# Kernel tuning notes

Measured on AMD Instinct MI355X. Metric: run time of the kernel, lower is better.

Reference implementation:

```python
import jax, jax.numpy as jnp
import numpy as np

N_NODES = 50000
N_EDGES = 640000
D_IN = 128
D_HID = 128
D_OUT = 128
N_GRAPHS = 64


def gcn_conv(x, edge_index, W, b, n_nodes):
    """PyG GCNConv: D^{-1/2} (A + I) D^{-1/2} X W + b (unit edge weights)."""
    src, dst = edge_index[0], edge_index[1]
    h = x @ W  # [N, d_out]
    # degree counts target-side edges plus the self loop
    deg = jax.ops.segment_sum(jnp.ones_like(dst, dtype=h.dtype), dst,
                              num_segments=n_nodes) + 1.0
    dinv = jax.lax.rsqrt(deg)  # deg >= 1 so always finite
    norm = dinv[src] * dinv[dst]  # [E]
    msg = h[src] * norm[:, None]  # gather + scale  [E, d_out]
    agg = jax.ops.segment_sum(msg, dst, num_segments=n_nodes)
    # self-loop contribution: norm_ii = dinv_i^2
    agg = agg + h * (dinv * dinv)[:, None]
    return agg + b


def global_mean_pool(x, batch, n_graphs):
    sums = jax.ops.segment_sum(x, batch, num_segments=n_graphs)
    cnt = jax.ops.segment_sum(jnp.ones((x.shape[0],), dtype=x.dtype), batch,
                              num_segments=n_graphs)
    return sums / jnp.maximum(cnt, 1.0)[:, None]


def setup_inputs() -> dict:
    key = jax.random.key(0)
    k = jax.random.split(key, 8)
    x = jax.random.normal(k[0], (N_NODES, D_IN), dtype=jnp.float32)
    edge_index = jax.random.randint(k[1], (2, N_EDGES), 0, N_NODES, dtype=jnp.int64)
    batch = jnp.sort(jax.random.randint(k[2], (N_NODES,), 0, N_GRAPHS, dtype=jnp.int64))
    s1 = 1.0 / np.sqrt(D_IN)
    s2 = 1.0 / np.sqrt(D_HID)
    W1 = jax.random.uniform(k[3], (D_IN, D_HID), jnp.float32, -s1, s1)
    b1 = jnp.zeros((D_HID,), jnp.float32)
    W2 = jax.random.uniform(k[4], (D_HID, D_OUT), jnp.float32, -s2, s2)
    b2 = jnp.zeros((D_OUT,), jnp.float32)
    return {"x": x, "edge_index": edge_index, "batch": batch,
            "W1": W1, "b1": b1, "W2": W2, "b2": b2}


def reference(x, edge_index, batch, W1, b1, W2, b2):
    n = x.shape[0]
    h = jax.nn.relu(gcn_conv(x, edge_index, W1, b1, n))
    h = gcn_conv(h, edge_index, W2, b2, n)
    return global_mean_pool(h, batch, N_GRAPHS)
```

## Files before the change

### kernel.cpp

```cpp
#include <hip/hip_runtime.h>


#define D 128
#define NGRAPH 64
#define AGG_BLOCKS 2048
#define BUCK_SH 9
#define BUCK_W  512
#define MAXBUCK 128

typedef _Float16 h16x2 __attribute__((ext_vector_type(2)));
typedef _Float16 f16x8 __attribute__((ext_vector_type(8)));
typedef float    f32x4 __attribute__((ext_vector_type(4)));
typedef unsigned short u16x8 __attribute__((ext_vector_type(8)));

__device__ __forceinline__ float2 h2f(unsigned u) {
    h16x2 h = __builtin_bit_cast(h16x2, u);
    return make_float2((float)h.x, (float)h.y);
}
__device__ __forceinline__ unsigned f2h(float x, float y) {
    h16x2 h;
    h.x = (_Float16)x;
    h.y = (_Float16)y;
    return __builtin_bit_cast(unsigned, h);
}
__device__ __forceinline__ void fmix2(float& ax, float& ay, unsigned u) {
    h16x2 h = __builtin_bit_cast(h16x2, u);
#if __has_builtin(__builtin_amdgcn_fdot2)
    const h16x2 onelo = {(_Float16)1.0f, (_Float16)0.0f};
    const h16x2 onehi = {(_Float16)0.0f, (_Float16)1.0f};
    ax = __builtin_amdgcn_fdot2(h, onelo, ax, false);
    ay = __builtin_amdgcn_fdot2(h, onehi, ay, false);
#else
    ax += (float)h.x;
    ay += (float)h.y;
#endif
}

__global__ void zero_out_kernel(float* __restrict__ out, int n) {
    int i = blockIdx.x * blockDim.x + threadIdx.x;
    if (i < n) out[i] = 0.f;
}

__global__ __launch_bounds__(256) void pack_scatter_kernel(const float* __restrict__ W1,
                                                           _Float16* __restrict__ WB,
                                                           const int* __restrict__ ei,
                                                           int* __restrict__ bcnt,
                                                           unsigned* __restrict__ buck,
                                                           unsigned* __restrict__ Gz,
                                                           unsigned* __restrict__ Hz,
                                                           int N, int E, int CAP) {
    int b = (int)blockIdx.x;
    int t = (int)threadIdx.x;
    if (b < 8) {
        int idx = b * 256 + t;
        int lane = idx & 63;
        int nt   = (idx >> 6) & 7;
        int kt   = idx >> 9;
        int col  = nt * 16 + (lane & 15);
        int krow = kt * 32 + (lane >> 4) * 8;
#pragma unroll
        for (int j = 0; j < 8; ++j)
            WB[idx * 8 + j] = (_Float16)W1[(krow + j) * D + col];
        return;
    }
    if (b == 8) {
        if (t < 64)       Gz[(size_t)N * 64 + t] = 0u;
        else if (t < 128) Hz[(size_t)N * 64 + (t - 64)] = 0u;
        return;
    }
    __shared__ unsigned histL[MAXBUCK];
    __shared__ int      baseL[MAXBUCK];
    if (t < MAXBUCK) histL[t] = 0u;
    __syncthreads();

    int e0 = (b - 9) * 1024;
    int bid[4];
    unsigned lidx[4], pk[4];
#pragma unroll
    for (int j = 0; j < 4; ++j) {
        int e = e0 + t + j * 256;
        bid[j] = -1;
        if (e < E) {
            int s = ei[e];
            int d = ei[E + e];
            if (d >= 0 && d < N) {
                s = min(max(s, 0), N - 1);
                bid[j] = d >> BUCK_SH;
                pk[j]  = ((unsigned)d << 16) | (unsigned)s;
            }
        }
    }
#pragma unroll
    for (int j = 0; j < 4; ++j)
        if (bid[j] >= 0) lidx[j] = atomicAdd(&histL[bid[j]], 1u);
    __syncthreads();
    if (t < MAXBUCK && histL[t] > 0u)
        baseL[t] = atomicAdd(&bcnt[t], (int)histL[t]);
    __syncthreads();
#pragma unroll
    for (int j = 0; j < 4; ++j)
        if (bid[j] >= 0) {
            int slot = baseL[bid[j]] + (int)lidx[j];
            if (slot < CAP) buck[(size_t)bid[j] * CAP + slot] = pk[j];
        }
}

__global__ __launch_bounds__(256) void bucket_deg_kernel(const unsigned* __restrict__ buck,
                                                         const int* __restrict__ bcnt,
                                                         int* __restrict__ deg,
                                                         float* __restrict__ dinv,
                                                         int* __restrict__ padsum,
                                                         int* __restrict__ bbase,
                                                         int* __restrict__ rowstart,
                                                         int* __restrict__ ticket,
                                                         int N, int CAP, int nbuck) {
    __shared__ int degL[BUCK_W];
    __shared__ int red[256];
    __shared__ int lastFlag;
    int b = (int)blockIdx.x;
    int t = (int)threadIdx.x;
    for (int k = t; k < BUCK_W; k += 256) degL[k] = 0;
    __syncthreads();
    int cnt = min(bcnt[b], CAP);
    const unsigned* bp = buck + (size_t)b * CAP;
    for (int i = t; i < cnt; i += 256)
        atomicAdd(&degL[(bp[i] >> 16) & (BUCK_W - 1)], 1);
    __syncthreads();
    int base = b << BUCK_SH;
    int local = 0;
    for (int k = t; k < BUCK_W; k += 256) {
        int d = base + k;
        if (d < N) {
            int dg = degL[k];
            deg[d]  = dg;
            dinv[d] = rsqrtf((float)dg + 1.0f);
            local  += (dg + 7) & ~7;
        }
    }
    red[t] = local;
    __syncthreads();
    for (int off = 128; off > 0; off >>= 1) {
        if (t < off) red[t] += red[t + off];
        __syncthreads();
    }
    if (t == 0) padsum[b] = red[0];
    __threadfence();
    if (t == 0) lastFlag = (atomicAdd(ticket, 1) == nbuck - 1) ? 1 : 0;
    __syncthreads();
    if (lastFlag) {
        __threadfence();
        __shared__ int s[128];
        int own = (t < nbuck) ? padsum[t] : 0;
        if (t < 128) s[t] = own;
        __syncthreads();
        for (int off = 1; off < 128; off <<= 1) {
            int v = (t < 128 && t >= off) ? s[t - off] : 0;
            __syncthreads();
            if (t < 128) s[t] += v;
            __syncthreads();
        }
        if (t < nbuck) bbase[t] = s[t] - own;
        if (t == 127) rowstart[N] = s[127];
    }
}

__global__ __launch_bounds__(256) void gemm_fill_kernel(const float* __restrict__ X,
                                                        const _Float16* __restrict__ WB,
                                                        const float* __restrict__ dinv,
                                                        _Float16* __restrict__ Gh,
                                                        const unsigned* __restrict__ buck,
                                                        const int* __restrict__ bcnt,
                                                        const int* __restrict__ deg,
                                                        const int* __restrict__ bbase,
                                                        int* __restrict__ rowstart,
                                                        unsigned short* __restrict__ colidx,
                                                        int N, int CAP, int gb) {
    if ((int)blockIdx.x >= gb) {
        __shared__ int degS[BUCK_W];
        __shared__ int loff[BUCK_W];
        __shared__ int sc[256];
        int b = (int)blockIdx.x - gb;
        int t = (int)threadIdx.x;
        int base_d = b << BUCK_SH;
        for (int k = t; k < BUCK_W; k += 256) {
            int d = base_d + k;
            degS[k] = (d < N) ? deg[d] : 0;
        }
        __syncthreads();
        int p0 = (degS[2 * t] + 7) & ~7;
        int p1 = (degS[2 * t + 1] + 7) & ~7;
        int own = p0 + p1;
        sc[t] = own;
        __syncthreads();
        for (int off = 1; off < 256; off <<= 1) {
            int v = (t >= off) ? sc[t - off] : 0;
            __syncthreads();
            sc[t] += v;
            __syncthreads();
        }
        int excl = sc[t] - own;
        loff[2 * t]     = excl;
        loff[2 * t + 1] = excl + p0;
        __syncthreads();
        int bb = bbase[b];
        for (int k = t; k < BUCK_W; k += 256) {
            int d = base_d + k;
            if (d < N) {
                int rs = bb + loff[k];
                rowstart[d] = rs;
                int dg = degS[k];
                int p8 = (dg + 7) & ~7;
                for (int j = dg; j < p8; ++j)
                    colidx[rs + j] = (unsigned short)N;
            }
        }
        __syncthreads();
        for (int k = t; k < BUCK_W; k += 256) degS[k] = bb + loff[k];
        __syncthreads();
        int cnt = min(bcnt[b], CAP);
        const unsigned* bp = buck + (size_t)b * CAP;
        for (int i = t; i < cnt; i += 256) {
            unsigned u = bp[i];
            int ld = (int)((u >> 16) & (BUCK_W - 1));
            int slot = atomicAdd(&degS[ld], 1);
            colidx[slot] = (unsigned short)(u & 0xffffu);
        }
        return;
    }

    int t = (int)threadIdx.x;
    int wave = t >> 6, lane = t & 63;
    int mbase = blockIdx.x * 64 + wave * 16;
    int arow  = mbase + (lane & 15);
    if (arow >= N) arow = N - 1;
    int kgrp  = lane >> 4;

    f16x8 afrag[4];
#pragma unroll
    for (int kt = 0; kt < 4; ++kt) {
        const float* xp = X + (size_t)arow * D + kt * 32 + kgrp * 8;
        float4 a0 = *(const float4*)xp;
        float4 a1 = *(const float4*)(xp + 4);
        f16x8 af;
        af[0] = (_Float16)a0.x; af[1] = (_Float16)a0.y;
        af[2] = (_Float16)a0.z; af[3] = (_Float16)a0.w;
        af[4] = (_Float16)a1.x; af[5] = (_Float16)a1.y;
        af[6] = (_Float16)a1.z; af[7] = (_Float16)a1.w;
        afrag[kt] = af;
    }
    f32x4 acc[8];
#pragma unroll
    for (int nt = 0; nt < 8; ++nt) acc[nt] = (f32x4){0.f, 0.f, 0.f, 0.f};
#pragma unroll
    for (int kt = 0; kt < 4; ++kt) {
#pragma unroll
        for (int nt = 0; nt < 8; ++nt) {
            uint4 u = *(const uint4*)(WB + (((kt * 8 + nt) * 64 + lane) * 8));
            f16x8 bfrag = __builtin_bit_cast(f16x8, u);
            acc[nt] = __builtin_amdgcn_mfma_f32_16x16x32_f16(afrag[kt], bfrag, acc[nt], 0, 0, 0);
        }
    }
    int r0 = mbase + kgrp * 4;
#pragma unroll
    for (int r = 0; r < 4; ++r) {
        int row = r0 + r;
        if (row < N) {
            float dv = dinv[row];
#pragma unroll
            for (int nt = 0; nt < 8; ++nt)
                Gh[(size_t)row * D + nt * 16 + (lane & 15)] = (_Float16)(dv * acc[nt][r]);
        }
    }
}

__global__ __launch_bounds__(256) void agg1_kernel(const unsigned* __restrict__ Gh,
                                                   const int* __restrict__ rowstart,
                                                   const unsigned short* __restrict__ colidx,
                                                   const float* __restrict__ dinv,
                                                   const float* __restrict__ b1,
                                                   unsigned* __restrict__ Hh,
                                                   int N, int chunk) {
    int gid  = blockIdx.x * 4 + (threadIdx.x >> 6);
    unsigned lane = threadIdx.x & 63;
    int i0 = gid * chunk, i1 = min(i0 + chunk, N);
    float bx = b1[2 * lane], by = b1[2 * lane + 1];
    for (int i = i0; i < i1; ++i) {
        float di = dinv[i];
        float ax = 0.f, ay = 0.f;
        fmix2(ax, ay, Gh[((unsigned)i << 6) + lane]);
        int e0 = rowstart[i], e1 = rowstart[i + 1];
        int e = e0;
        for (; e + 15 < e1; e += 16) {
            u16x8 c0 = *(const u16x8*)(colidx + e);
            u16x8 c1 = *(const u16x8*)(colidx + e + 8);
            unsigned u[16];
#pragma unroll
            for (int j = 0; j < 8; ++j)
                u[j] = Gh[((unsigned)c0[j] << 6) + lane];
#pragma unroll
            for (int j = 0; j < 8; ++j)
                u[8 + j] = Gh[((unsigned)c1[j] << 6) + lane];
#pragma unroll
            for (int j = 0; j < 16; ++j) fmix2(ax, ay, u[j]);
        }
        for (; e < e1; e += 8) {
            u16x8 cc = *(const u16x8*)(colidx + e);
            unsigned u[8];
#pragma unroll
            for (int j = 0; j < 8; ++j)
                u[j] = Gh[((unsigned)cc[j] << 6) + lane];
#pragma unroll
            for (int j = 0; j < 8; ++j) fmix2(ax, ay, u[j]);
        }
        float hx = fmaxf(fmaf(di, ax, bx), 0.f) * di;
        float hy = fmaxf(fmaf(di, ay, by), 0.f) * di;
        Hh[((unsigned)i << 6) + lane] = f2h(hx, hy);
    }
}

__global__ __launch_bounds__(256) void agg2_pool_kernel(const unsigned* __restrict__ Hh,
                                                        const int* __restrict__ rowstart,
                                                        const unsigned short* __restrict__ colidx,
                                                        const float* __restrict__ dinv,
                                                        const int* __restrict__ batch,
                                                        float* __restrict__ pool,
                                                        int N, int chunk) {
    int gid  = blockIdx.x * 4 + (threadIdx.x >> 6);
    unsigned lane = threadIdx.x & 63;
    int i0 = gid * chunk, i1 = min(i0 + chunk, N);
    if (i0 >= N) return;

    float2 pa = make_float2(0.f, 0.f);
    int cur = min(max(batch[i0], 0), NGRAPH - 1);
    for (int i = i0; i < i1; ++i) {
        float di = dinv[i];
        float ax = 0.f, ay = 0.f;
        fmix2(ax, ay, Hh[((unsigned)i << 6) + lane]);
        int e0 = rowstart[i], e1 = rowstart[i + 1];
        int e = e0;
        for (; e + 15 < e1; e += 16) {
            u16x8 c0 = *(const u16x8*)(colidx + e);
            u16x8 c1 = *(const u16x8*)(colidx + e + 8);
            unsigned u[16];
#pragma unroll
            for (int j = 0; j < 8; ++j)
                u[j] = Hh[((unsigned)c0[j] << 6) + lane];
#pragma unroll
            for (int j = 0; j < 8; ++j)
                u[8 + j] = Hh[((unsigned)c1[j] << 6) + lane];
#pragma unroll
            for (int j = 0; j < 16; ++j) fmix2(ax, ay, u[j]);
        }
        for (; e < e1; e += 8) {
            u16x8 cc = *(const u16x8*)(colidx + e);
            unsigned u[8];
#pragma unroll
            for (int j = 0; j < 8; ++j)
                u[j] = Hh[((unsigned)cc[j] << 6) + lane];
#pragma unroll
            for (int j = 0; j < 8; ++j) fmix2(ax, ay, u[j]);
        }
        int b = min(max(batch[i], 0), NGRAPH - 1);
        if (b != cur) {
            atomicAdd(&pool[(size_t)cur * D + 2 * lane], pa.x);
            atomicAdd(&pool[(size_t)cur * D + 2 * lane + 1], pa.y);
            pa = make_float2(0.f, 0.f);
            cur = b;
        }
        pa.x = fmaf(di, ax, pa.x);
        pa.y = fmaf(di, ay, pa.y);
    }
    atomicAdd(&pool[(size_t)cur * D + 2 * lane], pa.x);
    atomicAdd(&pool[(size_t)cur * D + 2 * lane + 1], pa.y);
}

__device__ __forceinline__ int lbound(const int* __restrict__ a, int n, int v) {
    int lo = 0, hi = n;
    while (lo < hi) {
        int m = (lo + hi) >> 1;
        if (a[m] < v) lo = m + 1; else hi = m;
    }
    return lo;
}

__global__ void final_gemm_kernel(const float* __restrict__ pool,
                                  const int* __restrict__ batch,
                                  const float* __restrict__ W2,
                                  const float* __restrict__ b2,
                                  float* __restrict__ out, int N) {
    int g = blockIdx.x, o = threadIdx.x;
    int s = lbound(batch, N, g);
    int e = lbound(batch, N, g + 1);
    float inv_cnt = 1.0f / fmaxf((float)(e - s), 1.0f);
    float acc = 0.f;
#pragma unroll 4
    for (int k = 0; k < D; ++k)
        acc = fmaf(pool[g * D + k], W2[k * D + o], acc);
    out[g * D + o] = acc * inv_cnt + b2[o];
}


extern "C" void kernel_launch(void* const* d_in, const int* in_sizes, int n_in,
                              void* d_out, int out_size, void* d_ws, size_t ws_size,
                              hipStream_t stream) {
    const float* x     = (const float*)d_in[0];
    const int*   ei    = (const int*)  d_in[1];
    const int*   batch = (const int*)  d_in[2];
    const float* W1    = (const float*)d_in[3];
    const float* b1    = (const float*)d_in[4];
    const float* W2    = (const float*)d_in[5];
    const float* b2    = (const float*)d_in[6];
    float* out = (float*)d_out;

    const int N = in_sizes[0] / D;
    const int E = in_sizes[1] / 2;
    const int nbuck = (N + BUCK_W - 1) >> BUCK_SH;
    const int CAP   = (E / (nbuck > 0 ? nbuck : 1)) * 2 + 1024;

    char* ws = (char*)d_ws;
    size_t off = 0;
    auto carve = [&](size_t bytes) {
        size_t o = off;
        off = (off + bytes + 255) & ~(size_t)255;
        return o;
    };
    size_t o_bcnt     = carve((size_t)MAXBUCK * 4);
    size_t o_pool     = carve((size_t)NGRAPH * D * 4);
    size_t o_ticket   = carve((size_t)256);
    size_t zspan      = off;
    size_t o_rowstart = carve((size_t)(N + 1) * 4);
    size_t o_deg      = carve((size_t)N * 4);
    size_t o_dinv     = carve((size_t)N * 4);
    size_t o_padsum   = carve((size_t)MAXBUCK * 4);
    size_t o_bbase    = carve((size_t)MAXBUCK * 4);
    size_t o_colidx   = carve(((size_t)E + 7 * (size_t)N + 64) * 2);
    size_t o_buck     = carve((size_t)nbuck * CAP * 4);
    size_t o_wb       = carve((size_t)D * D * 2);
    size_t o_gh       = carve((size_t)(N + 1) * D * 2);
    size_t o_hh       = carve((size_t)(N + 1) * D * 2);
    size_t need = off;

    if (ws_size < need) {
        zero_out_kernel<<<(out_size + 255) / 256, 256, 0, stream>>>(out, out_size);
        return;
    }

    int*            bcnt     = (int*)           (ws + o_bcnt);
    float*          pool     = (float*)         (ws + o_pool);
    int*            ticket   = (int*)           (ws + o_ticket);
    int*            rowstart = (int*)           (ws + o_rowstart);
    int*            deg      = (int*)           (ws + o_deg);
    float*          dinv     = (float*)         (ws + o_dinv);
    int*            padsum   = (int*)           (ws + o_padsum);
    int*            bbase    = (int*)           (ws + o_bbase);
    unsigned short* colidx   = (unsigned short*)(ws + o_colidx);
    unsigned*       buck     = (unsigned*)      (ws + o_buck);
    _Float16*       WB       = (_Float16*)      (ws + o_wb);
    _Float16*       Gh       = (_Float16*)      (ws + o_gh);
    _Float16*       Hh       = (_Float16*)      (ws + o_hh);

    hipMemsetAsync(ws, 0, zspan, stream);

    int ebs = (E + 1023) / 1024;
    int gb  = (N + 63) / 64;

    pack_scatter_kernel<<<9 + ebs, 256, 0, stream>>>(W1, WB, ei, bcnt, buck,
                                                     (unsigned*)Gh, (unsigned*)Hh,
                                                     N, E, CAP);
    bucket_deg_kernel<<<nbuck, 256, 0, stream>>>(buck, bcnt, deg, dinv, padsum,
                                                 bbase, rowstart, ticket,
                                                 N, CAP, nbuck);
    gemm_fill_kernel<<<gb + nbuck, 256, 0, stream>>>(x, WB, dinv, Gh, buck, bcnt,
                                                     deg, bbase, rowstart, colidx,
                                                     N, CAP, gb);

    int groups = AGG_BLOCKS * 4;
    int chunk  = (N + groups - 1) / groups;
    agg1_kernel<<<AGG_BLOCKS, 256, 0, stream>>>((const unsigned*)Gh, rowstart, colidx,
                                                dinv, b1, (unsigned*)Hh, N, chunk);
    agg2_pool_kernel<<<AGG_BLOCKS, 256, 0, stream>>>((const unsigned*)Hh, rowstart, colidx,
                                                     dinv, batch, pool, N, chunk);
    final_gemm_kernel<<<NGRAPH, D, 0, stream>>>(pool, batch, W2, b2, out, N);
}
```

Before: 201.4 us.

## Merge degree pass into CSR fill kernel with per-bucket flags and pad rows to 4

Removes the separate bucket_deg kernel. The bucket blocks of gemm_fill now count degrees themselves and use a fixed per-bucket colidx region (CAPQ), which drops the global prefix scan. Each GEMM block spins on a per-bucket flag before reading dinv, so the GEMM can overlap with CSR construction inside one launch. Row extents become int2 (start,end), padding drops from 8 to 4 with a 4-wide tail path, and the fdot2 accumulation is replaced with plain converts and adds. The spin-wait could deadlock if GEMM blocks are scheduled ahead of bucket blocks and fill the device, though bucket blocks have lower indices so they should be dispatched first.

```diff
diff --git a/kernel.cpp b/kernel.cpp
--- a/kernel.cpp
+++ b/kernel.cpp
@@ -12,6 +12,7 @@
 typedef _Float16 f16x8 __attribute__((ext_vector_type(8)));
 typedef float    f32x4 __attribute__((ext_vector_type(4)));
 typedef unsigned short u16x8 __attribute__((ext_vector_type(8)));
+typedef unsigned short u16x4 __attribute__((ext_vector_type(4)));
 
 __device__ __forceinline__ float2 h2f(unsigned u) {
     h16x2 h = __builtin_bit_cast(h16x2, u);
@@ -22,18 +23,6 @@
     h.x = (_Float16)x;
     h.y = (_Float16)y;
     return __builtin_bit_cast(unsigned, h);
-}
-__device__ __forceinline__ void fmix2(float& ax, float& ay, unsigned u) {
-    h16x2 h = __builtin_bit_cast(h16x2, u);
-#if __has_builtin(__builtin_amdgcn_fdot2)
-    const h16x2 onelo = {(_Float16)1.0f, (_Float16)0.0f};
-    const h16x2 onehi = {(_Float16)0.0f, (_Float16)1.0f};
-    ax = __builtin_amdgcn_fdot2(h, onelo, ax, false);
-    ay = __builtin_amdgcn_fdot2(h, onehi, ay, false);
-#else
-    ax += (float)h.x;
-    ay += (float)h.y;
-#endif
 }
 
 __global__ void zero_out_kernel(float* __restrict__ out, int n) {
@@ -105,90 +94,32 @@
         }
 }
 
-__global__ __launch_bounds__(256) void bucket_deg_kernel(const unsigned* __restrict__ buck,
-                                                         const int* __restrict__ bcnt,
-                                                         int* __restrict__ deg,
-                                                         float* __restrict__ dinv,
-                                                         int* __restrict__ padsum,
-                                                         int* __restrict__ bbase,
-                                                         int* __restrict__ rowstart,
-                                                         int* __restrict__ ticket,
-                                                         int N, int CAP, int nbuck) {
-    __shared__ int degL[BUCK_W];
-    __shared__ int red[256];
-    __shared__ int lastFlag;
-    int b = (int)blockIdx.x;
+__global__ __launch_bounds__(256, 4) void gemm_fill_kernel(const float* __restrict__ X,
+                                                           const _Float16* __restrict__ WB,
+                                                           const unsigned* __restrict__ buck,
+                                                           const int* __restrict__ bcnt,
+                                                           float* __restrict__ dinv,
+                                                           int2* __restrict__ rs2,
+                                                           unsigned short* __restrict__ colidx,
+                                                           int* __restrict__ flags,
+                                                           _Float16* __restrict__ Gh,
+                                                           int N, int CAP, int CAPQ, int nbuck) {
     int t = (int)threadIdx.x;
-    for (int k = t; k < BUCK_W; k += 256) degL[k] = 0;
-    __syncthreads();
-    int cnt = min(bcnt[b], CAP);
-    const unsigned* bp = buck + (size_t)b * CAP;
-    for (int i = t; i < cnt; i += 256)
-        atomicAdd(&degL[(bp[i] >> 16) & (BUCK_W - 1)], 1);
-    __syncthreads();
-    int base = b << BUCK_SH;
-    int local = 0;
-    for (int k = t; k < BUCK_W; k += 256) {
-        int d = base + k;
-        if (d < N) {
-            int dg = degL[k];
-            deg[d]  = dg;
-            dinv[d] = rsqrtf((float)dg + 1.0f);
-            local  += (dg + 7) & ~7;
-        }
-    }
-    red[t] = local;
-    __syncthreads();
-    for (int off = 128; off > 0; off >>= 1) {
-        if (t < off) red[t] += red[t + off];
-        __syncthreads();
-    }
-    if (t == 0) padsum[b] = red[0];
-    __threadfence();
-    if (t == 0) lastFlag = (atomicAdd(ticket, 1) == nbuck - 1) ? 1 : 0;
-    __syncthreads();
-    if (lastFlag) {
-        __threadfence();
-        __shared__ int s[128];
-        int own = (t < nbuck) ? padsum[t] : 0;
-        if (t < 128) s[t] = own;
-        __syncthreads();
-        for (int off = 1; off < 128; off <<= 1) {
-            int v = (t < 128 && t >= off) ? s[t - off] : 0;
-            __syncthreads();
-            if (t < 128) s[t] += v;
-            __syncthreads();
-        }
-        if (t < nbuck) bbase[t] = s[t] - own;
-        if (t == 127) rowstart[N] = s[127];
-    }
-}
-
-__global__ __launch_bounds__(256) void gemm_fill_kernel(const float* __restrict__ X,
-                                                        const _Float16* __restrict__ WB,
-                                                        const float* __restrict__ dinv,
-                                                        _Float16* __restrict__ Gh,
-                                                        const unsigned* __restrict__ buck,
-                                                        const int* __restrict__ bcnt,
-                                                        const int* __restrict__ deg,
-                                                        const int* __restrict__ bbase,
-                                                        int* __restrict__ rowstart,
-                                                        unsigned short* __restrict__ colidx,
-                                                        int N, int CAP, int gb) {
-    if ((int)blockIdx.x >= gb) {
+    if ((int)blockIdx.x < nbuck) {
         __shared__ int degS[BUCK_W];
         __shared__ int loff[BUCK_W];
         __shared__ int sc[256];
-        int b = (int)blockIdx.x - gb;
-        int t = (int)threadIdx.x;
-        int base_d = b << BUCK_SH;
-        for (int k = t; k < BUCK_W; k += 256) {
-            int d = base_d + k;
-            degS[k] = (d < N) ? deg[d] : 0;
-        }
-        __syncthreads();
-        int p0 = (degS[2 * t] + 7) & ~7;
-        int p1 = (degS[2 * t + 1] + 7) & ~7;
+        int b = (int)blockIdx.x;
+        for (int k = t; k < BUCK_W; k += 256) degS[k] = 0;
+        __syncthreads();
+        int cnt = min(bcnt[b], CAP);
+        const unsigned* bp = buck + (size_t)b * CAP;
+        for (int i = t; i < cnt; i += 256)
+            atomicAdd(&degS[(bp[i] >> 16) & (BUCK_W - 1)], 1);
+        __syncthreads();
+        int d0 = degS[2 * t], d1 = degS[2 * t + 1];
+        int p0 = (d0 + 7) & ~7;
+        int p1 = (d1 + 7) & ~7;
         int own = p0 + p1;
         sc[t] = own;
         __syncthreads();
@@ -202,23 +133,28 @@
         loff[2 * t]     = excl;
         loff[2 * t + 1] = excl + p0;
         __syncthreads();
-        int bb = bbase[b];
+        int BB = b * CAPQ;
+        int base_d = b << BUCK_SH;
         for (int k = t; k < BUCK_W; k += 256) {
             int d = base_d + k;
             if (d < N) {
-                int rs = bb + loff[k];
-                rowstart[d] = rs;
                 int dg = degS[k];
-                int p8 = (dg + 7) & ~7;
-                for (int j = dg; j < p8; ++j)
+                int rs = BB + loff[k];
+                int p4 = (dg + 3) & ~3;
+                __hip_atomic_store(&dinv[d], rsqrtf((float)dg + 1.0f),
+                                   __ATOMIC_RELAXED, __HIP_MEMORY_SCOPE_AGENT);
+                rs2[d] = make_int2(rs, rs + p4);
+                for (int j = dg; j < p4; ++j)
                     colidx[rs + j] = (unsigned short)N;
             }
         }
         __syncthreads();
-        for (int k = t; k < BUCK_W; k += 256) degS[k] = bb + loff[k];
-        __syncthreads();
-        int cnt = min(bcnt[b], CAP);
-        const unsigned* bp = buck + (size_t)b * CAP;
+        if (t == 0) {
+            __threadfence();
+            atomicExch(&flags[b], 1);
+        }
+        for (int k = t; k < BUCK_W; k += 256) degS[k] = BB + loff[k];
+        __syncthreads();
         for (int i = t; i < cnt; i += 256) {
             unsigned u = bp[i];
             int ld = (int)((u >> 16) & (BUCK_W - 1));
@@ -228,9 +164,9 @@
         return;
     }
 
-    int t = (int)threadIdx.x;
+    int gbid = (int)blockIdx.x - nbuck;
     int wave = t >> 6, lane = t & 63;
-    int mbase = blockIdx.x * 64 + wave * 16;
+    int mbase = gbid * 64 + wave * 16;
     int arow  = mbase + (lane & 15);
     if (arow >= N) arow = N - 1;
     int kgrp  = lane >> 4;
@@ -260,12 +196,20 @@
             acc[nt] = __builtin_amdgcn_mfma_f32_16x16x32_f16(afrag[kt], bfrag, acc[nt], 0, 0, 0);
         }
     }
+    int mybuck = gbid >> 3;
+    if (mybuck >= nbuck) mybuck = nbuck - 1;
+    if (t == 0) {
+        while (atomicAdd(&flags[mybuck], 0) == 0) __builtin_amdgcn_s_sleep(16);
+        __threadfence();
+    }
+    __syncthreads();
     int r0 = mbase + kgrp * 4;
 #pragma unroll
     for (int r = 0; r < 4; ++r) {
         int row = r0 + r;
         if (row < N) {
-            float dv = dinv[row];
+            float dv = __hip_atomic_load(&dinv[row], __ATOMIC_RELAXED,
+                                         __HIP_MEMORY_SCOPE_AGENT);
 #pragma unroll
             for (int nt = 0; nt < 8; ++nt)
                 Gh[(size_t)row * D + nt * 16 + (lane & 15)] = (_Float16)(dv * acc[nt][r]);
@@ -274,7 +218,7 @@
 }
 
 __global__ __launch_bounds__(256) void agg1_kernel(const unsigned* __restrict__ Gh,
-                                                   const int* __restrict__ rowstart,
+                                                   const int2* __restrict__ rs2,
                                                    const unsigned short* __restrict__ colidx,
                                                    const float* __restrict__ dinv,
                                                    const float* __restrict__ b1,
@@ -286,10 +230,10 @@
     float bx = b1[2 * lane], by = b1[2 * lane + 1];
     for (int i = i0; i < i1; ++i) {
         float di = dinv[i];
-        float ax = 0.f, ay = 0.f;
-        fmix2(ax, ay, Gh[((unsigned)i << 6) + lane]);
-        int e0 = rowstart[i], e1 = rowstart[i + 1];
-        int e = e0;
+        float2 s = h2f(Gh[((unsigned)i << 6) + lane]);
+        float ax = s.x, ay = s.y;
+        int2 se = rs2[i];
+        int e = se.x, e1 = se.y;
         for (; e + 15 < e1; e += 16) {
             u16x8 c0 = *(const u16x8*)(colidx + e);
             u16x8 c1 = *(const u16x8*)(colidx + e + 8);
@@ -301,16 +245,38 @@
             for (int j = 0; j < 8; ++j)
                 u[8 + j] = Gh[((unsigned)c1[j] << 6) + lane];
 #pragma unroll
-            for (int j = 0; j < 16; ++j) fmix2(ax, ay, u[j]);
-        }
-        for (; e < e1; e += 8) {
+            for (int j = 0; j < 16; ++j) {
+                float2 v = h2f(u[j]);
+                ax += v.x;
+                ay += v.y;
+            }
+        }
+        if (e + 7 < e1) {
             u16x8 cc = *(const u16x8*)(colidx + e);
             unsigned u[8];
 #pragma unroll
             for (int j = 0; j < 8; ++j)
                 u[j] = Gh[((unsigned)cc[j] << 6) + lane];
 #pragma unroll
-            for (int j = 0; j < 8; ++j) fmix2(ax, ay, u[j]);
+            for (int j = 0; j < 8; ++j) {
+                float2 v = h2f(u[j]);
+                ax += v.x;
+                ay += v.y;
+            }
+            e += 8;
+        }
+        if (e + 3 < e1) {
+            u16x4 cc = *(const u16x4*)(colidx + e);
+            unsigned u[4];
+#pragma unroll
+            for (int j = 0; j < 4; ++j)
+                u[j] = Gh[((unsigned)cc[j] << 6) + lane];
+#pragma unroll
+            for (int j = 0; j < 4; ++j) {
+                float2 v = h2f(u[j]);
+                ax += v.x;
+                ay += v.y;
+            }
         }
         float hx = fmaxf(fmaf(di, ax, bx), 0.f) * di;
         float hy = fmaxf(fmaf(di, ay, by), 0.f) * di;
@@ -319,7 +285,7 @@
 }
 
 __global__ __launch_bounds__(256) void agg2_pool_kernel(const unsigned* __restrict__ Hh,
-                                                        const int* __restrict__ rowstart,
+                                                        const int2* __restrict__ rs2,
                                                         const unsigned short* __restrict__ colidx,
                                                         const float* __restrict__ dinv,
                                                         const int* __restrict__ batch,
@@ -334,10 +300,10 @@
     int cur = min(max(batch[i0], 0), NGRAPH - 1);
     for (int i = i0; i < i1; ++i) {
         float di = dinv[i];
-        float ax = 0.f, ay = 0.f;
-        fmix2(ax, ay, Hh[((unsigned)i << 6) + lane]);
-        int e0 = rowstart[i], e1 = rowstart[i + 1];
-        int e = e0;
+        float2 s = h2f(Hh[((unsigned)i << 6) + lane]);
+        float ax = s.x, ay = s.y;
+        int2 se = rs2[i];
+        int e = se.x, e1 = se.y;
         for (; e + 15 < e1; e += 16) {
             u16x8 c0 = *(const u16x8*)(colidx + e);
             u16x8 c1 = *(const u16x8*)(colidx + e + 8);
@@ -349,16 +315,38 @@
             for (int j = 0; j < 8; ++j)
                 u[8 + j] = Hh[((unsigned)c1[j] << 6) + lane];
 #pragma unroll
-            for (int j = 0; j < 16; ++j) fmix2(ax, ay, u[j]);
-        }
-        for (; e < e1; e += 8) {
+            for (int j = 0; j < 16; ++j) {
+                float2 v = h2f(u[j]);
+                ax += v.x;
+                ay += v.y;
+            }
+        }
+        if (e + 7 < e1) {
             u16x8 cc = *(const u16x8*)(colidx + e);
             unsigned u[8];
 #pragma unroll
             for (int j = 0; j < 8; ++j)
                 u[j] = Hh[((unsigned)cc[j] << 6) + lane];
 #pragma unroll
-            for (int j = 0; j < 8; ++j) fmix2(ax, ay, u[j]);
+            for (int j = 0; j < 8; ++j) {
+                float2 v = h2f(u[j]);
+                ax += v.x;
+                ay += v.y;
+            }
+            e += 8;
+        }
+        if (e + 3 < e1) {
+            u16x4 cc = *(const u16x4*)(colidx + e);
+            unsigned u[4];
+#pragma unroll
+            for (int j = 0; j < 4; ++j)
+                u[j] = Hh[((unsigned)cc[j] << 6) + lane];
+#pragma unroll
+            for (int j = 0; j < 4; ++j) {
+                float2 v = h2f(u[j]);
+                ax += v.x;
+                ay += v.y;
+            }
         }
         int b = min(max(batch[i], 0), NGRAPH - 1);
         if (b != cur) {
@@ -416,6 +404,7 @@
     const int E = in_sizes[1] / 2;
     const int nbuck = (N + BUCK_W - 1) >> BUCK_SH;
     const int CAP   = (E / (nbuck > 0 ? nbuck : 1)) * 2 + 1024;
+    const int CAPQ  = CAP + 8 * BUCK_W;
 
     char* ws = (char*)d_ws;
     size_t off = 0;
@@ -426,14 +415,11 @@
     };
     size_t o_bcnt     = carve((size_t)MAXBUCK * 4);
     size_t o_pool     = carve((size_t)NGRAPH * D * 4);
-    size_t o_ticket   = carve((size_t)256);
+    size_t o_flags    = carve((size_t)MAXBUCK * 4);
     size_t zspan      = off;
-    size_t o_rowstart = carve((size_t)(N + 1) * 4);
-    size_t o_deg      = carve((size_t)N * 4);
+    size_t o_rs2      = carve((size_t)N * 8);
     size_t o_dinv     = carve((size_t)N * 4);
-    size_t o_padsum   = carve((size_t)MAXBUCK * 4);
-    size_t o_bbase    = carve((size_t)MAXBUCK * 4);
-    size_t o_colidx   = carve(((size_t)E + 7 * (size_t)N + 64) * 2);
+    size_t o_colidx   = carve((size_t)nbuck * CAPQ * 2);
     size_t o_buck     = carve((size_t)nbuck * CAP * 4);
     size_t o_wb       = carve((size_t)D * D * 2);
     size_t o_gh       = carve((size_t)(N + 1) * D * 2);
@@ -447,12 +433,9 @@
 
     int*            bcnt     = (int*)           (ws + o_bcnt);
     float*          pool     = (float*)         (ws + o_pool);
-    int*            ticket   = (int*)           (ws + o_ticket);
-    int*            rowstart = (int*)           (ws + o_rowstart);
-    int*            deg      = (int*)           (ws + o_deg);
+    int*            flags    = (int*)           (ws + o_flags);
+    int2*           rs2      = (int2*)          (ws + o_rs2);
     float*          dinv     = (float*)         (ws + o_dinv);
-    int*            padsum   = (int*)           (ws + o_padsum);
-    int*            bbase    = (int*)           (ws + o_bbase);
     unsigned short* colidx   = (unsigned short*)(ws + o_colidx);
     unsigned*       buck     = (unsigned*)      (ws + o_buck);
     _Float16*       WB       = (_Float16*)      (ws + o_wb);
@@ -467,18 +450,15 @@
     pack_scatter_kernel<<<9 + ebs, 256, 0, stream>>>(W1, WB, ei, bcnt, buck,
                                                      (unsigned*)Gh, (unsigned*)Hh,
                                                      N, E, CAP);
-    bucket_deg_kernel<<<nbuck, 256, 0, stream>>>(buck, bcnt, deg, dinv, padsum,
-                                                 bbase, rowstart, ticket,
-                                                 N, CAP, nbuck);
-    gemm_fill_kernel<<<gb + nbuck, 256, 0, stream>>>(x, WB, dinv, Gh, buck, bcnt,
-                                                     deg, bbase, rowstart, colidx,
-                                                     N, CAP, gb);
+    gemm_fill_kernel<<<nbuck + gb, 256, 0, stream>>>(x, WB, buck, bcnt, dinv, rs2,
+                                                     colidx, flags, Gh,
+                                                     N, CAP, CAPQ, nbuck);
 
     int groups = AGG_BLOCKS * 4;
     int chunk  = (N + groups - 1) / groups;
-    agg1_kernel<<<AGG_BLOCKS, 256, 0, stream>>>((const unsigned*)Gh, rowstart, colidx,
+    agg1_kernel<<<AGG_BLOCKS, 256, 0, stream>>>((const unsigned*)Gh, rs2, colidx,
                                                 dinv, b1, (unsigned*)Hh, N, chunk);
-    agg2_pool_kernel<<<AGG_BLOCKS, 256, 0, stream>>>((const unsigned*)Hh, rowstart, colidx,
+    agg2_pool_kernel<<<AGG_BLOCKS, 256, 0, stream>>>((const unsigned*)Hh, rs2, colidx,
                                                      dinv, batch, pool, N, chunk);
     final_gemm_kernel<<<NGRAPH, D, 0, stream>>>(pool, batch, W2, b2, out, N);
 }
```

New measurement: 213.9 us. 1.06x slower.
